# Performance work log

Hardware: AMD Instinct MI355X
Metric: run time of the kernel (lower is better)

The kernel has to match this reference:

```python
import jax, jax.numpy as jnp
import numpy as np

N_TARGETS = 4
BATCH_SIZE = 4
B = N_TARGETS * BATCH_SIZE
N_SAMPLES = 1024
LAYERS = [(128, 128), (256, 64), (512, 32)]  # (channels, spatial)
EPS_COS = 1e-10


def setup_inputs() -> dict:
    key = jax.random.key(0)
    inp = {}
    for l, (c, s) in enumerate(LAYERS):
        k1, k2, k3, k4, key = jax.random.split(key, 5)
        n = s * s
        inp[f't{l}'] = jax.random.normal(k1, (N_TARGETS, c, s, s), dtype=jnp.float32)
        inp[f'g{l}'] = jax.random.normal(k2, (B, c, s, s), dtype=jnp.float32)
        inp[f'ix{l}'] = jax.random.randint(k3, (B, N_SAMPLES), 0, n)
        inp[f'iy{l}'] = jax.random.randint(k4, (B, N_SAMPLES), 0, n)
    return inp


def _cos_remd(x, y):
    # x: (b,n,c), y: (b,m,c)
    xn = jnp.linalg.norm(x, axis=2, keepdims=True)            # (b,n,1)
    yn = jnp.linalg.norm(y, axis=2, keepdims=True)            # (b,m,1)
    cross = jnp.einsum('bnc,bmc->bnm', x, y)                  # (b,n,m)
    dist = 1.0 - cross / (xn * yn.transpose(0, 2, 1) + EPS_COS)
    m1 = dist.min(axis=1).mean(axis=1)                        # min over n, mean over m
    m2 = dist.min(axis=2).mean(axis=1)                        # min over m, mean over n
    return jnp.maximum(m1, m2)                                # (b,)


def _moment_loss(x, y):
    mu_x = x.mean(axis=1, keepdims=True)
    mu_y = y.mean(axis=1, keepdims=True)
    mu_diff = jnp.abs(mu_x - mu_y).mean(axis=(1, 2))
    x_c = x - mu_x
    y_c = y - mu_y
    x_cov = jnp.einsum('bnc,bnd->bcd', x_c, x_c) / (x.shape[1] - 1)
    y_cov = jnp.einsum('bmc,bmd->bcd', y_c, y_c) / (y.shape[1] - 1)
    cov_diff = jnp.abs(x_cov - y_cov).mean(axis=(1, 2))
    return mu_diff + cov_diff                                 # (b,)


def _layer_loss(t, g, ix, iy):
    b, c, h, w = g.shape
    y = jnp.tile(t, (BATCH_SIZE, 1, 1, 1)).reshape(b, t.shape[1], -1)  # (b,c,n_y)
    x = g.reshape(b, c, -1)                                            # (b,c,n_x)
    x = jnp.take_along_axis(x, ix[:, None, :], axis=2)                 # (b,c,ns)
    y = jnp.take_along_axis(y, iy[:, None, :], axis=2)                 # (b,c,ns)
    x = x.transpose(0, 2, 1)
    y = y.transpose(0, 2, 1)
    return _cos_remd(x, y) + _moment_loss(x, y)


def reference(t0, g0, t1, g1, t2, g2, ix0, iy0, ix1, iy1, ix2, iy2):
    loss = (_layer_loss(t0, g0, ix0, iy0)
            + _layer_loss(t1, g1, ix1, iy1)
            + _layer_loss(t2, g2, ix2, iy2))
    return loss.reshape(BATCH_SIZE, N_TARGETS).mean(axis=0)   # (n_targets,)
```

## Files before the change

### kernel.cpp

```cpp
#include <hip/hip_runtime.h>
#include <math.h>

#define NT 4
#define BSZ 4
#define BB 16
#define NS 1024
#define CCH 32
#define MAXL 3

typedef unsigned short u16;
typedef __attribute__((ext_vector_type(8))) short bf16x8;
typedef __attribute__((ext_vector_type(4))) float f32x4;

struct LayerP {
    const float *g, *t;
    const int *ix, *iy;
    u16 *Xt, *Yt, *Xn, *Yn;
    float *xp, *yp, *xnv, *ynv, *sx, *sy;
    unsigned *m1u, *m2u;
    float *cov;
    int C, n, nchunk, ntri, lid;
};
struct Tab {
    LayerP L[MAXL];
    int nl, nb, b0;
    float* losspart;
};

__device__ __forceinline__ unsigned fenc(float f) {
    unsigned u = __float_as_uint(f);
    return (u & 0x80000000u) ? ~u : (u | 0x80000000u);
}
__device__ __forceinline__ float fdec(unsigned u) {
    unsigned v = (u & 0x80000000u) ? (u & 0x7FFFFFFFu) : ~u;
    return __uint_as_float(v);
}
__device__ __forceinline__ u16 f2bf(float f) {
    unsigned u = __float_as_uint(f);
    unsigned r = u + 0x7FFFu + ((u >> 16) & 1u);
    return (u16)(r >> 16);
}
__device__ __forceinline__ float bf2f(u16 h) {
    return __uint_as_float((unsigned)h << 16);
}

__global__ void gather_t(Tab tab)
{
    int x = blockIdx.x, l = 0;
    while (l < MAXL - 1 && x >= tab.L[l].C) { x -= tab.L[l].C; ++l; }
    const LayerP P = tab.L[l];
    int c = x, bl = blockIdx.y, bg = tab.b0 + bl;
    int tid = threadIdx.x;
    const float* __restrict__ grow = P.g + ((size_t)bg * P.C + c) * P.n;
    const float* __restrict__ trow = P.t + ((size_t)(bg % NT) * P.C + c) * P.n;
    const int* __restrict__ ixr = P.ix + bg * NS;
    const int* __restrict__ iyr = P.iy + bg * NS;
    u16* __restrict__ xo = P.Xt + ((size_t)bl * P.C + c) * NS;
    u16* __restrict__ yo = P.Yt + ((size_t)bl * P.C + c) * NS;
    float ax = 0.f, ay = 0.f;
    #pragma unroll
    for (int rep = 0; rep < NS / 256; ++rep) {
        int s = tid + rep * 256;
        u16 xb = f2bf(grow[ixr[s]]);
        u16 yb = f2bf(trow[iyr[s]]);
        xo[s] = xb;
        yo[s] = yb;
        ax += bf2f(xb);
        ay += bf2f(yb);
    }
    __shared__ float red[2][4];
    for (int o = 32; o > 0; o >>= 1) { ax += __shfl_down(ax, o); ay += __shfl_down(ay, o); }
    int wid = tid >> 6, lane = tid & 63;
    if (lane == 0) { red[0][wid] = ax; red[1][wid] = ay; }
    __syncthreads();
    if (tid == 0) {
        P.sx[bl * P.C + c] = red[0][0] + red[0][1] + red[0][2] + red[0][3];
        P.sy[bl * P.C + c] = red[1][0] + red[1][1] + red[1][2] + red[1][3];
    }
}

__global__ void colnorm_part(Tab tab)
{
    int y = blockIdx.y, l = 0;
    while (l < MAXL - 1 && y >= tab.L[l].nchunk) { y -= tab.L[l].nchunk; ++l; }
    const LayerP P = tab.L[l];
    int chunk = y, bl = blockIdx.z;
    int s2 = blockIdx.x * 512 + threadIdx.x * 2;
    size_t base = ((size_t)bl * P.C + (size_t)chunk * CCH) * NS + s2;
    const u16* __restrict__ Xt = P.Xt;
    const u16* __restrict__ Yt = P.Yt;
    float ax0 = 0.f, ax1 = 0.f, ay0 = 0.f, ay1 = 0.f;
    #pragma unroll 8
    for (int c = 0; c < CCH; ++c) {
        unsigned xv = *(const unsigned*)&Xt[base + (size_t)c * NS];
        unsigned yv = *(const unsigned*)&Yt[base + (size_t)c * NS];
        float x0 = bf2f((u16)xv), x1 = bf2f((u16)(xv >> 16));
        float y0 = bf2f((u16)yv), y1 = bf2f((u16)(yv >> 16));
        ax0 = fmaf(x0, x0, ax0); ax1 = fmaf(x1, x1, ax1);
        ay0 = fmaf(y0, y0, ay0); ay1 = fmaf(y1, y1, ay1);
    }
    size_t o = ((size_t)bl * P.nchunk + chunk) * NS + s2;
    *(float2*)&P.xp[o] = make_float2(ax0, ax1);
    *(float2*)&P.yp[o] = make_float2(ay0, ay1);
}

__global__ void colnorm_reduce(Tab tab)
{
    const LayerP P = tab.L[blockIdx.y];
    int bl = blockIdx.z;
    int s = blockIdx.x * 256 + threadIdx.x;
    float ax = 0.f, ay = 0.f;
    for (int k = 0; k < P.nchunk; ++k) {
        size_t o = ((size_t)bl * P.nchunk + k) * NS + s;
        ax += P.xp[o];
        ay += P.yp[o];
    }
    P.xnv[bl * NS + s] = sqrtf(ax);
    P.ynv[bl * NS + s] = sqrtf(ay);
    P.m1u[bl * NS + s] = 0xFFFFFFFFu;
    P.m2u[bl * NS + s] = 0xFFFFFFFFu;
}

__global__ void transpose_norm(Tab tab)
{
    int x = blockIdx.x, l = 0;
    while (l < MAXL - 1 && x >= tab.L[l].C / 64) { x -= tab.L[l].C / 64; ++l; }
    const LayerP P = tab.L[l];
    int z = blockIdx.z;
    int bl = z >> 1, which = z & 1;
    const u16* __restrict__ Zt = which ? P.Yt : P.Xt;
    const float* __restrict__ zn = which ? P.ynv : P.xnv;
    u16* __restrict__ Zn = which ? P.Yn : P.Xn;
    int C = P.C;
    int c0 = x * 64, s0 = blockIdx.y * 64;
    __shared__ __align__(16) u16 T[64][72];
    int tid = threadIdx.x;
    #pragma unroll
    for (int rep = 0; rep < 2; ++rep) {
        int q = tid + rep * 256;
        int rr = q >> 3, seg = q & 7;
        *(float4*)&T[rr][seg * 8] =
            *(const float4*)&Zt[((size_t)bl * C + c0 + rr) * NS + s0 + seg * 8];
    }
    __syncthreads();
    #pragma unroll
    for (int rep = 0; rep < 2; ++rep) {
        int q = tid + rep * 256;
        int sr = q >> 3, cs = q & 7;
        float inv = 1.0f / zn[bl * NS + s0 + sr];
        __align__(16) u16 tmp[8];
        #pragma unroll
        for (int e = 0; e < 8; ++e) tmp[e] = f2bf(bf2f(T[cs * 8 + e][sr]) * inv);
        *(float4*)&Zn[((size_t)bl * NS + s0 + sr) * C + c0 + cs * 8] = *(float4*)tmp;
    }
}

__global__ __launch_bounds__(256) void cross_mfma(Tab tab)
{
    int z = blockIdx.z;
    int l = z / tab.nb, bl = z - l * tab.nb;
    const LayerP P = tab.L[l];
    int C = P.C;
    int i0 = blockIdx.x * 128, j0 = blockIdx.y * 128;
    __shared__ __align__(16) u16 As[128][40], Bs[128][40];
    int tid = threadIdx.x;
    int w = tid >> 6, lane = tid & 63;
    int wr = w >> 1, wc = w & 1;
    int q = lane >> 4, r = lane & 15;
    const u16* __restrict__ Xb = P.Xn + ((size_t)bl * NS + i0) * C;
    const u16* __restrict__ Yb = P.Yn + ((size_t)bl * NS + j0) * C;
    f32x4 acc[4][4];
    #pragma unroll
    for (int m = 0; m < 4; ++m)
        #pragma unroll
        for (int nn = 0; nn < 4; ++nn) acc[m][nn] = (f32x4){0.f, 0.f, 0.f, 0.f};

    for (int kk = 0; kk < C; kk += 32) {
        __syncthreads();
        #pragma unroll
        for (int rep = 0; rep < 2; ++rep) {
            int qid = tid + rep * 256;
            int row = qid >> 2, seg = qid & 3;
            size_t off = (size_t)row * C + kk + seg * 8;
            *(float4*)&As[row][seg * 8] = *(const float4*)&Xb[off];
            *(float4*)&Bs[row][seg * 8] = *(const float4*)&Yb[off];
        }
        __syncthreads();
        bf16x8 a[4], b[4];
        #pragma unroll
        for (int m = 0; m < 4; ++m)
            a[m] = *(const bf16x8*)&As[wr * 64 + m * 16 + r][q * 8];
        #pragma unroll
        for (int nn = 0; nn < 4; ++nn)
            b[nn] = *(const bf16x8*)&Bs[wc * 64 + nn * 16 + r][q * 8];
        #pragma unroll
        for (int m = 0; m < 4; ++m)
            #pragma unroll
            for (int nn = 0; nn < 4; ++nn)
                acc[m][nn] = __builtin_amdgcn_mfma_f32_16x16x32_bf16(a[m], b[nn], acc[m][nn], 0, 0, 0);
    }

    float rm[4][4], cm[4];
    #pragma unroll
    for (int m = 0; m < 4; ++m)
        #pragma unroll
        for (int reg = 0; reg < 4; ++reg) rm[m][reg] = 1e30f;
    #pragma unroll
    for (int nn = 0; nn < 4; ++nn) cm[nn] = 1e30f;
    #pragma unroll
    for (int m = 0; m < 4; ++m)
        #pragma unroll
        for (int nn = 0; nn < 4; ++nn)
            #pragma unroll
            for (int reg = 0; reg < 4; ++reg) {
                float d = 1.f - acc[m][nn][reg];
                rm[m][reg] = fminf(rm[m][reg], d);
                cm[nn] = fminf(cm[nn], d);
            }
    #pragma unroll
    for (int m = 0; m < 4; ++m)
        #pragma unroll
        for (int reg = 0; reg < 4; ++reg) {
            float v = rm[m][reg];
            v = fminf(v, __shfl_xor(v, 1));
            v = fminf(v, __shfl_xor(v, 2));
            v = fminf(v, __shfl_xor(v, 4));
            v = fminf(v, __shfl_xor(v, 8));
            rm[m][reg] = v;
        }
    if (r == 0) {
        #pragma unroll
        for (int m = 0; m < 4; ++m)
            #pragma unroll
            for (int reg = 0; reg < 4; ++reg) {
                int i = i0 + wr * 64 + m * 16 + q * 4 + reg;
                atomicMin(&P.m2u[bl * NS + i], fenc(rm[m][reg]));
            }
    }
    #pragma unroll
    for (int nn = 0; nn < 4; ++nn) {
        float v = cm[nn];
        v = fminf(v, __shfl_xor(v, 16));
        v = fminf(v, __shfl_xor(v, 32));
        cm[nn] = v;
    }
    if (q == 0) {
        #pragma unroll
        for (int nn = 0; nn < 4; ++nn) {
            int j = j0 + wc * 64 + nn * 16 + r;
            atomicMin(&P.m1u[bl * NS + j], fenc(cm[nn]));
        }
    }
}

__global__ __launch_bounds__(256) void cov_mfma(Tab tab)
{
    int x = blockIdx.x, l = 0;
    while (l < MAXL - 1 && x >= tab.L[l].ntri) { x -= tab.L[l].ntri; ++l; }
    const LayerP P = tab.L[l];
    int u = x;
    int bl = blockIdx.y;
    int C = P.C;
    int ty = 0;
    while ((ty + 1) * (ty + 2) / 2 <= u) ++ty;
    int tx = u - ty * (ty + 1) / 2;
    int c0 = ty * 128, d0 = tx * 128;
    float wgt = (tx == ty) ? 1.f : 2.f;

    __shared__ __align__(16) u16 As[128][40], Bs[128][40], Cs2[128][40], Ds[128][40];
    int tid = threadIdx.x;
    int w = tid >> 6, lane = tid & 63;
    int wr = w >> 1, wc = w & 1;
    int q = lane >> 4, r = lane & 15;
    const u16* __restrict__ Xc = P.Xt + ((size_t)bl * C + c0) * NS;
    const u16* __restrict__ Xd = P.Xt + ((size_t)bl * C + d0) * NS;
    const u16* __restrict__ Yc = P.Yt + ((size_t)bl * C + c0) * NS;
    const u16* __restrict__ Yd = P.Yt + ((size_t)bl * C + d0) * NS;

    f32x4 accX[4][4], accY[4][4];
    #pragma unroll
    for (int m = 0; m < 4; ++m)
        #pragma unroll
        for (int nn = 0; nn < 4; ++nn) {
            accX[m][nn] = (f32x4){0.f, 0.f, 0.f, 0.f};
            accY[m][nn] = (f32x4){0.f, 0.f, 0.f, 0.f};
        }

    for (int ss = 0; ss < NS; ss += 32) {
        __syncthreads();
        #pragma unroll
        for (int rep = 0; rep < 2; ++rep) {
            int qid = tid + rep * 256;
            int row = qid >> 2, seg = qid & 3;
            size_t off = (size_t)row * NS + ss + seg * 8;
            *(float4*)&As[row][seg * 8]  = *(const float4*)&Xc[off];
            *(float4*)&Bs[row][seg * 8]  = *(const float4*)&Xd[off];
            *(float4*)&Cs2[row][seg * 8] = *(const float4*)&Yc[off];
            *(float4*)&Ds[row][seg * 8]  = *(const float4*)&Yd[off];
        }
        __syncthreads();
        {
            bf16x8 a[4], b[4];
            #pragma unroll
            for (int m = 0; m < 4; ++m) a[m] = *(const bf16x8*)&As[wr * 64 + m * 16 + r][q * 8];
            #pragma unroll
            for (int nn = 0; nn < 4; ++nn) b[nn] = *(const bf16x8*)&Bs[wc * 64 + nn * 16 + r][q * 8];
            #pragma unroll
            for (int m = 0; m < 4; ++m)
                #pragma unroll
                for (int nn = 0; nn < 4; ++nn)
                    accX[m][nn] = __builtin_amdgcn_mfma_f32_16x16x32_bf16(a[m], b[nn], accX[m][nn], 0, 0, 0);
        }
        {
            bf16x8 a[4], b[4];
            #pragma unroll
            for (int m = 0; m < 4; ++m) a[m] = *(const bf16x8*)&Cs2[wr * 64 + m * 16 + r][q * 8];
            #pragma unroll
            for (int nn = 0; nn < 4; ++nn) b[nn] = *(const bf16x8*)&Ds[wc * 64 + nn * 16 + r][q * 8];
            #pragma unroll
            for (int m = 0; m < 4; ++m)
                #pragma unroll
                for (int nn = 0; nn < 4; ++nn)
                    accY[m][nn] = __builtin_amdgcn_mfma_f32_16x16x32_bf16(a[m], b[nn], accY[m][nn], 0, 0, 0);
        }
    }

    float scxv[4][4], scyv[4][4], sdxv[4], sdyv[4];
    #pragma unroll
    for (int m = 0; m < 4; ++m)
        #pragma unroll
        for (int reg = 0; reg < 4; ++reg) {
            int c = c0 + wr * 64 + m * 16 + q * 4 + reg;
            scxv[m][reg] = P.sx[bl * C + c];
            scyv[m][reg] = P.sy[bl * C + c];
        }
    #pragma unroll
    for (int nn = 0; nn < 4; ++nn) {
        int d = d0 + wc * 64 + nn * 16 + r;
        sdxv[nn] = P.sx[bl * C + d];
        sdyv[nn] = P.sy[bl * C + d];
    }
    const float invNS = 1.f / NS, invNSm1 = 1.f / (NS - 1);
    float tsum = 0.f;
    #pragma unroll
    for (int m = 0; m < 4; ++m)
        #pragma unroll
        for (int nn = 0; nn < 4; ++nn)
            #pragma unroll
            for (int reg = 0; reg < 4; ++reg) {
                float cx = (accX[m][nn][reg] - scxv[m][reg] * sdxv[nn] * invNS) * invNSm1;
                float cy = (accY[m][nn][reg] - scyv[m][reg] * sdyv[nn] * invNS) * invNSm1;
                tsum += fabsf(cx - cy);
            }
    tsum *= wgt;
    __shared__ float redc[4];
    for (int o = 32; o > 0; o >>= 1) tsum += __shfl_down(tsum, o);
    if (lane == 0) redc[w] = tsum;
    __syncthreads();
    if (tid == 0)
        P.cov[(size_t)bl * P.ntri + u] = redc[0] + redc[1] + redc[2] + redc[3];
}

__global__ void finalize_kernel(Tab tab)
{
    const LayerP P = tab.L[blockIdx.x];
    int bl = blockIdx.y;
    int tid = threadIdx.x;
    int C = P.C;
    float s1 = 0.f, s2 = 0.f, smu = 0.f, scov = 0.f;
    for (int s = tid; s < NS; s += 256) {
        s1 += fdec(P.m1u[bl * NS + s]);
        s2 += fdec(P.m2u[bl * NS + s]);
    }
    for (int c = tid; c < C; c += 256) smu += fabsf(P.sx[bl * C + c] - P.sy[bl * C + c]);
    for (int i = tid; i < P.ntri; i += 256) scov += P.cov[(size_t)bl * P.ntri + i];
    __shared__ float red[4][4];
    for (int o = 32; o > 0; o >>= 1) {
        s1 += __shfl_down(s1, o);
        s2 += __shfl_down(s2, o);
        smu += __shfl_down(smu, o);
        scov += __shfl_down(scov, o);
    }
    int wid = tid >> 6, lane = tid & 63;
    if (lane == 0) { red[0][wid] = s1; red[1][wid] = s2; red[2][wid] = smu; red[3][wid] = scov; }
    __syncthreads();
    if (tid == 0) {
        s1 = red[0][0] + red[0][1] + red[0][2] + red[0][3];
        s2 = red[1][0] + red[1][1] + red[1][2] + red[1][3];
        smu = red[2][0] + red[2][1] + red[2][2] + red[2][3];
        scov = red[3][0] + red[3][1] + red[3][2] + red[3][3];
        float m1m = s1 * (1.f / NS), m2m = s2 * (1.f / NS);
        float mu_diff = smu * (1.f / NS) * (1.f / (float)C);
        float cov_diff = scov / ((float)C * (float)C);
        tab.losspart[(tab.b0 + bl) * 3 + P.lid] = fmaxf(m1m, m2m) + mu_diff + cov_diff;
    }
}

__global__ void out_kernel(const float* __restrict__ lp, float* __restrict__ out)
{
    int t = threadIdx.x;
    if (t < NT) {
        float s = 0.f;
        for (int k = 0; k < BSZ; ++k)
            for (int l = 0; l < 3; ++l)
                s += lp[(k * NT + t) * 3 + l];
        out[t] = s * (1.f / BSZ);
    }
}

static inline size_t alignup(size_t v) { return (v + 255) & ~(size_t)255; }

static size_t layer_bytes(int C, int nb) {
    int nchunk = C / CCH;
    int tc = C / 128, ntri = tc * (tc + 1) / 2;
    size_t szZ = alignup((size_t)NS * C * 2);
    size_t szP = alignup((size_t)nchunk * NS * 4);
    return (size_t)nb * (4 * szZ + 2 * szP + 4 * alignup(NS * 4)
                         + 2 * alignup(C * 4) + alignup(ntri * 4));
}

static char* fill_layer(LayerP& P, char* p, int C, int n, int nb, int lid,
                        const float* g, const float* t, const int* ix, const int* iy) {
    P.g = g; P.t = t; P.ix = ix; P.iy = iy;
    P.C = C; P.n = n; P.lid = lid;
    P.nchunk = C / CCH;
    int tc = C / 128;
    P.ntri = tc * (tc + 1) / 2;
    size_t szZ = alignup((size_t)NS * C * 2);
    size_t szP = alignup((size_t)P.nchunk * NS * 4);
    P.Xt = (u16*)p;  p += nb * szZ;
    P.Yt = (u16*)p;  p += nb * szZ;
    P.Xn = (u16*)p;  p += nb * szZ;
    P.Yn = (u16*)p;  p += nb * szZ;
    P.xp = (float*)p; p += nb * szP;
    P.yp = (float*)p; p += nb * szP;
    P.xnv = (float*)p; p += nb * alignup(NS * 4);
    P.ynv = (float*)p; p += nb * alignup(NS * 4);
    P.m1u = (unsigned*)p; p += nb * alignup(NS * 4);
    P.m2u = (unsigned*)p; p += nb * alignup(NS * 4);
    P.sx = (float*)p; p += nb * alignup(C * 4);
    P.sy = (float*)p; p += nb * alignup(C * 4);
    P.cov = (float*)p; p += nb * alignup(P.ntri * 4);
    return p;
}

static void launch_group(const Tab& tab, hipStream_t stream) {
    int sumC = 0, sumNchunk = 0, sumC64 = 0, sumNtri = 0;
    for (int l = 0; l < tab.nl; ++l) {
        sumC += tab.L[l].C;
        sumNchunk += tab.L[l].nchunk;
        sumC64 += tab.L[l].C / 64;
        sumNtri += tab.L[l].ntri;
    }
    int nb = tab.nb;
    gather_t<<<dim3(sumC, nb), 256, 0, stream>>>(tab);
    colnorm_part<<<dim3(NS / 512, sumNchunk, nb), 256, 0, stream>>>(tab);
    colnorm_reduce<<<dim3(NS / 256, tab.nl, nb), 256, 0, stream>>>(tab);
    transpose_norm<<<dim3(sumC64, NS / 64, nb * 2), 256, 0, stream>>>(tab);
    cross_mfma<<<dim3(NS / 128, NS / 128, tab.nl * nb), 256, 0, stream>>>(tab);
    cov_mfma<<<dim3(sumNtri, nb), 256, 0, stream>>>(tab);
    finalize_kernel<<<dim3(tab.nl, nb), 256, 0, stream>>>(tab);
}

extern "C" void kernel_launch(void* const* d_in, const int* in_sizes, int n_in,
                              void* d_out, int out_size, void* d_ws, size_t ws_size,
                              hipStream_t stream)
{
    const float* tp[3] = {(const float*)d_in[0], (const float*)d_in[4], (const float*)d_in[8]};
    const float* gp[3] = {(const float*)d_in[1], (const float*)d_in[5], (const float*)d_in[9]};
    const int* ixp[3]  = {(const int*)d_in[2], (const int*)d_in[6], (const int*)d_in[10]};
    const int* iyp[3]  = {(const int*)d_in[3], (const int*)d_in[7], (const int*)d_in[11]};
    const int Cs[3] = {128, 256, 512};
    const int Sp[3] = {128, 64, 32};

    float* out = (float*)d_out;
    char* ws = (char*)d_ws;
    float* losspart = (float*)ws;
    size_t base = alignup(BB * 3 * 4);
    size_t avail = (ws_size > base) ? ws_size - base : 0;

    size_t need_all = 0;
    for (int l = 0; l < 3; ++l) need_all += layer_bytes(Cs[l], BB);

    if (avail >= need_all) {
        Tab tab;
        tab.nl = 3; tab.nb = BB; tab.b0 = 0; tab.losspart = losspart;
        char* p = ws + base;
        for (int l = 0; l < 3; ++l)
            p = fill_layer(tab.L[l], p, Cs[l], Sp[l] * Sp[l], BB, l,
                           gp[l], tp[l], ixp[l], iyp[l]);
        launch_group(tab, stream);
    } else {
        for (int l = 0; l < 3; ++l) {
            size_t per_b = layer_bytes(Cs[l], 1);
            int G = (int)(avail / per_b);
            if (G > BB) G = BB;
            if (G < 1) G = 1;
            for (int b0 = 0; b0 < BB; b0 += G) {
                int nb = (BB - b0 < G) ? (BB - b0) : G;
                Tab tab;
                tab.nl = 1; tab.nb = nb; tab.b0 = b0; tab.losspart = losspart;
                fill_layer(tab.L[0], ws + base, Cs[l], Sp[l] * Sp[l], nb, l,
                           gp[l], tp[l], ixp[l], iyp[l]);
                launch_group(tab, stream);
            }
        }
    }
    out_kernel<<<1, 64, 0, stream>>>(losspart, out);
}
```

Measured before the change: 254.1 us.

## Stage gathers through LDS, share target rows, fuse norms into transpose

The gather is split into separate x and y kernels. Each one streams the full source channel row into shared memory in coalesced chunks and then picks the sampled elements from LDS, instead of doing random global loads. The y gather serves all four batch entries that share a target in one block, so each target row is read once. The per-column squared norms are now computed inside the transpose kernel, which removes the colnorm_part pass. Normalization moves to the cross-GEMM epilogue using reciprocal square roots, so the GEMM runs on unnormalized bf16 data and rounding may differ slightly. The cost is that every gather block reads the whole row (up to 16K floats) rather than only 1024 sampled points.

```diff
diff --git a/kernel.cpp b/kernel.cpp
--- a/kernel.cpp
+++ b/kernel.cpp
@@ -5,7 +5,7 @@
 #define BSZ 4
 #define BB 16
 #define NS 1024
-#define CCH 32
+#define GCH 4096
 #define MAXL 3
 
 typedef unsigned short u16;
@@ -15,15 +15,17 @@
 struct LayerP {
     const float *g, *t;
     const int *ix, *iy;
-    u16 *Xt, *Yt, *Xn, *Yn;
-    float *xp, *yp, *xnv, *ynv, *sx, *sy;
+    u16 *Xt, *Yt, *Xs, *Ys;
+    float *xp, *yp;
+    float *rxn, *ryn;
+    float *sx, *sy;
     unsigned *m1u, *m2u;
     float *cov;
     int C, n, nchunk, ntri, lid;
 };
 struct Tab {
     LayerP L[MAXL];
-    int nl, nb, b0;
+    int nl, nb, b0, ysh;
     float* losspart;
 };
 
@@ -44,7 +46,7 @@
     return __uint_as_float((unsigned)h << 16);
 }
 
-__global__ void gather_t(Tab tab)
+__global__ __launch_bounds__(256) void gather_x(Tab tab)
 {
     int x = blockIdx.x, l = 0;
     while (l < MAXL - 1 && x >= tab.L[l].C) { x -= tab.L[l].C; ++l; }
@@ -52,56 +54,150 @@
     int c = x, bl = blockIdx.y, bg = tab.b0 + bl;
     int tid = threadIdx.x;
     const float* __restrict__ grow = P.g + ((size_t)bg * P.C + c) * P.n;
-    const float* __restrict__ trow = P.t + ((size_t)(bg % NT) * P.C + c) * P.n;
     const int* __restrict__ ixr = P.ix + bg * NS;
-    const int* __restrict__ iyr = P.iy + bg * NS;
+    __shared__ __align__(16) float buf[GCH];
+    __shared__ float red[4];
+    int px[4];
+    float xv[4] = {0.f, 0.f, 0.f, 0.f};
+    #pragma unroll
+    for (int r = 0; r < 4; ++r) px[r] = ixr[tid + r * 256];
+    int n = P.n;
+    for (int lo = 0; lo < n; lo += GCH) {
+        int sz = min(GCH, n - lo);
+        __syncthreads();
+        for (int i = tid * 4; i < sz; i += 1024)
+            *(float4*)&buf[i] = *(const float4*)&grow[lo + i];
+        __syncthreads();
+        #pragma unroll
+        for (int r = 0; r < 4; ++r) {
+            int rel = px[r] - lo;
+            if ((unsigned)rel < (unsigned)sz) xv[r] = buf[rel];
+        }
+    }
     u16* __restrict__ xo = P.Xt + ((size_t)bl * P.C + c) * NS;
-    u16* __restrict__ yo = P.Yt + ((size_t)bl * P.C + c) * NS;
-    float ax = 0.f, ay = 0.f;
-    #pragma unroll
-    for (int rep = 0; rep < NS / 256; ++rep) {
-        int s = tid + rep * 256;
-        u16 xb = f2bf(grow[ixr[s]]);
-        u16 yb = f2bf(trow[iyr[s]]);
-        xo[s] = xb;
-        yo[s] = yb;
-        ax += bf2f(xb);
-        ay += bf2f(yb);
-    }
-    __shared__ float red[2][4];
-    for (int o = 32; o > 0; o >>= 1) { ax += __shfl_down(ax, o); ay += __shfl_down(ay, o); }
+    float ax = 0.f;
+    #pragma unroll
+    for (int r = 0; r < 4; ++r) {
+        u16 hb = f2bf(xv[r]);
+        xo[tid + r * 256] = hb;
+        ax += bf2f(hb);
+    }
+    for (int o = 32; o > 0; o >>= 1) ax += __shfl_down(ax, o);
     int wid = tid >> 6, lane = tid & 63;
-    if (lane == 0) { red[0][wid] = ax; red[1][wid] = ay; }
+    if (lane == 0) red[wid] = ax;
     __syncthreads();
-    if (tid == 0) {
-        P.sx[bl * P.C + c] = red[0][0] + red[0][1] + red[0][2] + red[0][3];
-        P.sy[bl * P.C + c] = red[1][0] + red[1][1] + red[1][2] + red[1][3];
-    }
-}
-
-__global__ void colnorm_part(Tab tab)
-{
-    int y = blockIdx.y, l = 0;
-    while (l < MAXL - 1 && y >= tab.L[l].nchunk) { y -= tab.L[l].nchunk; ++l; }
+    if (tid == 0) P.sx[bl * P.C + c] = red[0] + red[1] + red[2] + red[3];
+}
+
+__global__ __launch_bounds__(256) void gather_y(Tab tab)
+{
+    int x = blockIdx.x, l = 0;
+    while (l < MAXL - 1 && x >= tab.L[l].C) { x -= tab.L[l].C; ++l; }
     const LayerP P = tab.L[l];
-    int chunk = y, bl = blockIdx.z;
-    int s2 = blockIdx.x * 512 + threadIdx.x * 2;
-    size_t base = ((size_t)bl * P.C + (size_t)chunk * CCH) * NS + s2;
-    const u16* __restrict__ Xt = P.Xt;
-    const u16* __restrict__ Yt = P.Yt;
-    float ax0 = 0.f, ax1 = 0.f, ay0 = 0.f, ay1 = 0.f;
-    #pragma unroll 8
-    for (int c = 0; c < CCH; ++c) {
-        unsigned xv = *(const unsigned*)&Xt[base + (size_t)c * NS];
-        unsigned yv = *(const unsigned*)&Yt[base + (size_t)c * NS];
-        float x0 = bf2f((u16)xv), x1 = bf2f((u16)(xv >> 16));
-        float y0 = bf2f((u16)yv), y1 = bf2f((u16)(yv >> 16));
-        ax0 = fmaf(x0, x0, ax0); ax1 = fmaf(x1, x1, ax1);
-        ay0 = fmaf(y0, y0, ay0); ay1 = fmaf(y1, y1, ay1);
-    }
-    size_t o = ((size_t)bl * P.nchunk + chunk) * NS + s2;
-    *(float2*)&P.xp[o] = make_float2(ax0, ax1);
-    *(float2*)&P.yp[o] = make_float2(ay0, ay1);
+    int c = x, grp = blockIdx.y;
+    int tid = threadIdx.x;
+    int nk, tgt, bls[4];
+    if (tab.ysh == NT) {
+        nk = 4; tgt = grp;
+        #pragma unroll
+        for (int k = 0; k < 4; ++k) bls[k] = grp + NT * k;
+    } else {
+        nk = 1; bls[0] = grp; tgt = (tab.b0 + grp) % NT;
+        bls[1] = bls[2] = bls[3] = 0;
+    }
+    const float* __restrict__ trow = P.t + ((size_t)tgt * P.C + c) * P.n;
+    __shared__ __align__(16) float buf[GCH];
+    __shared__ float red[4][4];
+    int py[4][4];
+    float yv[4][4];
+    #pragma unroll
+    for (int k = 0; k < 4; ++k) {
+        if (k < nk) {
+            const int* iyr = P.iy + (tab.b0 + bls[k]) * NS;
+            #pragma unroll
+            for (int r = 0; r < 4; ++r) { py[k][r] = iyr[tid + r * 256]; yv[k][r] = 0.f; }
+        }
+    }
+    int n = P.n;
+    for (int lo = 0; lo < n; lo += GCH) {
+        int sz = min(GCH, n - lo);
+        __syncthreads();
+        for (int i = tid * 4; i < sz; i += 1024)
+            *(float4*)&buf[i] = *(const float4*)&trow[lo + i];
+        __syncthreads();
+        #pragma unroll
+        for (int k = 0; k < 4; ++k)
+            if (k < nk) {
+                #pragma unroll
+                for (int r = 0; r < 4; ++r) {
+                    int rel = py[k][r] - lo;
+                    if ((unsigned)rel < (unsigned)sz) yv[k][r] = buf[rel];
+                }
+            }
+    }
+    int wid = tid >> 6, lane = tid & 63;
+    #pragma unroll
+    for (int k = 0; k < 4; ++k) {
+        if (k >= nk) break;
+        u16* __restrict__ yo = P.Yt + ((size_t)bls[k] * P.C + c) * NS;
+        float ay = 0.f;
+        #pragma unroll
+        for (int r = 0; r < 4; ++r) {
+            u16 hb = f2bf(yv[k][r]);
+            yo[tid + r * 256] = hb;
+            ay += bf2f(hb);
+        }
+        for (int o = 32; o > 0; o >>= 1) ay += __shfl_down(ay, o);
+        if (lane == 0) red[k][wid] = ay;
+    }
+    __syncthreads();
+    if (tid < nk)
+        P.sy[bls[tid] * P.C + c] = red[tid][0] + red[tid][1] + red[tid][2] + red[tid][3];
+}
+
+__global__ void transpose_k(Tab tab)
+{
+    int x = blockIdx.x, l = 0;
+    while (l < MAXL - 1 && x >= tab.L[l].C / 64) { x -= tab.L[l].C / 64; ++l; }
+    const LayerP P = tab.L[l];
+    int z = blockIdx.z;
+    int bl = z >> 1, which = z & 1;
+    const u16* __restrict__ Zt = which ? P.Yt : P.Xt;
+    u16* __restrict__ Zs = which ? P.Ys : P.Xs;
+    float* __restrict__ zp = which ? P.yp : P.xp;
+    int C = P.C;
+    int ctile = x;
+    int c0 = ctile * 64, s0 = blockIdx.y * 64;
+    __shared__ __align__(16) u16 T[64][72];
+    int tid = threadIdx.x;
+    #pragma unroll
+    for (int rep = 0; rep < 2; ++rep) {
+        int q = tid + rep * 256;
+        int rr = q >> 3, seg = q & 7;
+        *(float4*)&T[rr][seg * 8] =
+            *(const float4*)&Zt[((size_t)bl * C + c0 + rr) * NS + s0 + seg * 8];
+    }
+    __syncthreads();
+    #pragma unroll
+    for (int rep = 0; rep < 2; ++rep) {
+        int q = tid + rep * 256;
+        int sr = q >> 3, cs = q & 7;
+        __align__(16) u16 tmp[8];
+        float p = 0.f;
+        #pragma unroll
+        for (int e = 0; e < 8; ++e) {
+            u16 h = T[cs * 8 + e][sr];
+            tmp[e] = h;
+            float v = bf2f(h);
+            p = fmaf(v, v, p);
+        }
+        *(float4*)&Zs[((size_t)bl * NS + s0 + sr) * C + c0 + cs * 8] = *(float4*)tmp;
+        p += __shfl_xor(p, 1);
+        p += __shfl_xor(p, 2);
+        p += __shfl_xor(p, 4);
+        if (cs == 0)
+            zp[((size_t)bl * P.nchunk + ctile) * NS + s0 + sr] = p;
+    }
 }
 
 __global__ void colnorm_reduce(Tab tab)
@@ -115,44 +211,10 @@
         ax += P.xp[o];
         ay += P.yp[o];
     }
-    P.xnv[bl * NS + s] = sqrtf(ax);
-    P.ynv[bl * NS + s] = sqrtf(ay);
+    P.rxn[bl * NS + s] = rsqrtf(ax);
+    P.ryn[bl * NS + s] = rsqrtf(ay);
     P.m1u[bl * NS + s] = 0xFFFFFFFFu;
     P.m2u[bl * NS + s] = 0xFFFFFFFFu;
-}
-
-__global__ void transpose_norm(Tab tab)
-{
-    int x = blockIdx.x, l = 0;
-    while (l < MAXL - 1 && x >= tab.L[l].C / 64) { x -= tab.L[l].C / 64; ++l; }
-    const LayerP P = tab.L[l];
-    int z = blockIdx.z;
-    int bl = z >> 1, which = z & 1;
-    const u16* __restrict__ Zt = which ? P.Yt : P.Xt;
-    const float* __restrict__ zn = which ? P.ynv : P.xnv;
-    u16* __restrict__ Zn = which ? P.Yn : P.Xn;
-    int C = P.C;
-    int c0 = x * 64, s0 = blockIdx.y * 64;
-    __shared__ __align__(16) u16 T[64][72];
-    int tid = threadIdx.x;
-    #pragma unroll
-    for (int rep = 0; rep < 2; ++rep) {
-        int q = tid + rep * 256;
-        int rr = q >> 3, seg = q & 7;
-        *(float4*)&T[rr][seg * 8] =
-            *(const float4*)&Zt[((size_t)bl * C + c0 + rr) * NS + s0 + seg * 8];
-    }
-    __syncthreads();
-    #pragma unroll
-    for (int rep = 0; rep < 2; ++rep) {
-        int q = tid + rep * 256;
-        int sr = q >> 3, cs = q & 7;
-        float inv = 1.0f / zn[bl * NS + s0 + sr];
-        __align__(16) u16 tmp[8];
-        #pragma unroll
-        for (int e = 0; e < 8; ++e) tmp[e] = f2bf(bf2f(T[cs * 8 + e][sr]) * inv);
-        *(float4*)&Zn[((size_t)bl * NS + s0 + sr) * C + c0 + cs * 8] = *(float4*)tmp;
-    }
 }
 
 __global__ __launch_bounds__(256) void cross_mfma(Tab tab)
@@ -167,8 +229,8 @@
     int w = tid >> 6, lane = tid & 63;
     int wr = w >> 1, wc = w & 1;
     int q = lane >> 4, r = lane & 15;
-    const u16* __restrict__ Xb = P.Xn + ((size_t)bl * NS + i0) * C;
-    const u16* __restrict__ Yb = P.Yn + ((size_t)bl * NS + j0) * C;
+    const u16* __restrict__ Xb = P.Xs + ((size_t)bl * NS + i0) * C;
+    const u16* __restrict__ Yb = P.Ys + ((size_t)bl * NS + j0) * C;
     f32x4 acc[4][4];
     #pragma unroll
     for (int m = 0; m < 4; ++m)
@@ -200,6 +262,16 @@
                 acc[m][nn] = __builtin_amdgcn_mfma_f32_16x16x32_bf16(a[m], b[nn], acc[m][nn], 0, 0, 0);
     }
 
+    float rxl[4][4], ryl[4];
+    #pragma unroll
+    for (int m = 0; m < 4; ++m)
+        #pragma unroll
+        for (int reg = 0; reg < 4; ++reg)
+            rxl[m][reg] = P.rxn[bl * NS + i0 + wr * 64 + m * 16 + q * 4 + reg];
+    #pragma unroll
+    for (int nn = 0; nn < 4; ++nn)
+        ryl[nn] = P.ryn[bl * NS + j0 + wc * 64 + nn * 16 + r];
+
     float rm[4][4], cm[4];
     #pragma unroll
     for (int m = 0; m < 4; ++m)
@@ -213,7 +285,7 @@
         for (int nn = 0; nn < 4; ++nn)
             #pragma unroll
             for (int reg = 0; reg < 4; ++reg) {
-                float d = 1.f - acc[m][nn][reg];
+                float d = 1.f - acc[m][nn][reg] * rxl[m][reg] * ryl[nn];
                 rm[m][reg] = fminf(rm[m][reg], d);
                 cm[nn] = fminf(cm[nn], d);
             }
@@ -411,7 +483,7 @@
 static inline size_t alignup(size_t v) { return (v + 255) & ~(size_t)255; }
 
 static size_t layer_bytes(int C, int nb) {
-    int nchunk = C / CCH;
+    int nchunk = C / 64;
     int tc = C / 128, ntri = tc * (tc + 1) / 2;
     size_t szZ = alignup((size_t)NS * C * 2);
     size_t szP = alignup((size_t)nchunk * NS * 4);
@@ -423,19 +495,19 @@
                         const float* g, const float* t, const int* ix, const int* iy) {
     P.g = g; P.t = t; P.ix = ix; P.iy = iy;
     P.C = C; P.n = n; P.lid = lid;
-    P.nchunk = C / CCH;
+    P.nchunk = C / 64;
     int tc = C / 128;
     P.ntri = tc * (tc + 1) / 2;
     size_t szZ = alignup((size_t)NS * C * 2);
     size_t szP = alignup((size_t)P.nchunk * NS * 4);
     P.Xt = (u16*)p;  p += nb * szZ;
     P.Yt = (u16*)p;  p += nb * szZ;
-    P.Xn = (u16*)p;  p += nb * szZ;
-    P.Yn = (u16*)p;  p += nb * szZ;
+    P.Xs = (u16*)p;  p += nb * szZ;
+    P.Ys = (u16*)p;  p += nb * szZ;
     P.xp = (float*)p; p += nb * szP;
     P.yp = (float*)p; p += nb * szP;
-    P.xnv = (float*)p; p += nb * alignup(NS * 4);
-    P.ynv = (float*)p; p += nb * alignup(NS * 4);
+    P.rxn = (float*)p; p += nb * alignup(NS * 4);
+    P.ryn = (float*)p; p += nb * alignup(NS * 4);
     P.m1u = (unsigned*)p; p += nb * alignup(NS * 4);
     P.m2u = (unsigned*)p; p += nb * alignup(NS * 4);
     P.sx = (float*)p; p += nb * alignup(C * 4);
@@ -445,18 +517,18 @@
 }
 
 static void launch_group(const Tab& tab, hipStream_t stream) {
-    int sumC = 0, sumNchunk = 0, sumC64 = 0, sumNtri = 0;
+    int sumC = 0, sumC64 = 0, sumNtri = 0;
     for (int l = 0; l < tab.nl; ++l) {
         sumC += tab.L[l].C;
-        sumNchunk += tab.L[l].nchunk;
         sumC64 += tab.L[l].C / 64;
         sumNtri += tab.L[l].ntri;
     }
     int nb = tab.nb;
-    gather_t<<<dim3(sumC, nb), 256, 0, stream>>>(tab);
-    colnorm_part<<<dim3(NS / 512, sumNchunk, nb), 256, 0, stream>>>(tab);
+    int ygrid = (tab.ysh == NT) ? NT : nb;
+    gather_x<<<dim3(sumC, nb), 256, 0, stream>>>(tab);
+    gather_y<<<dim3(sumC, ygrid), 256, 0, stream>>>(tab);
+    transpose_k<<<dim3(sumC64, NS / 64, nb * 2), 256, 0, stream>>>(tab);
     colnorm_reduce<<<dim3(NS / 256, tab.nl, nb), 256, 0, stream>>>(tab);
-    transpose_norm<<<dim3(sumC64, NS / 64, nb * 2), 256, 0, stream>>>(tab);
     cross_mfma<<<dim3(NS / 128, NS / 128, tab.nl * nb), 256, 0, stream>>>(tab);
     cov_mfma<<<dim3(sumNtri, nb), 256, 0, stream>>>(tab);
     finalize_kernel<<<dim3(tab.nl, nb), 256, 0, stream>>>(tab);
@@ -484,7 +556,7 @@
 
     if (avail >= need_all) {
         Tab tab;
-        tab.nl = 3; tab.nb = BB; tab.b0 = 0; tab.losspart = losspart;
+        tab.nl = 3; tab.nb = BB; tab.b0 = 0; tab.ysh = NT; tab.losspart = losspart;
         char* p = ws + base;
         for (int l = 0; l < 3; ++l)
             p = fill_layer(tab.L[l], p, Cs[l], Sp[l] * Sp[l], BB, l,
@@ -499,7 +571,7 @@
             for (int b0 = 0; b0 < BB; b0 += G) {
                 int nb = (BB - b0 < G) ? (BB - b0) : G;
                 Tab tab;
-                tab.nl = 1; tab.nb = nb; tab.b0 = b0; tab.losspart = losspart;
+                tab.nl = 1; tab.nb = nb; tab.b0 = b0; tab.ysh = 1; tab.losspart = losspart;
                 fill_layer(tab.L[0], ws + base, Cs[l], Sp[l] * Sp[l], nb, l,
                            gp[l], tp[l], ixp[l], iyp[l]);
                 launch_group(tab, stream);
```

Measured after the change: 230.5 us. -9.3%, faster.
